# Optimization experiments

Measured on AMD Instinct MI355X. Metric: run time of the kernel, lower is better.

The kernel has to match this reference:

```python
import jax, jax.numpy as jnp
import numpy as np
import math

TAU_MEM = 20.0
ALPHA = math.exp(-1.0 / TAU_MEM)
BASE_THRESHOLD = 1.0


def setup_inputs() -> dict:
    key = jax.random.key(0)
    k1, k2, k3 = jax.random.split(key, 3)
    B, T, D, H = 32, 1024, 512, 512
    x = jax.random.normal(k1, (B, T, D), dtype=jnp.float32)
    # nn.Linear default init: U(-1/sqrt(D), 1/sqrt(D))
    bound = 1.0 / math.sqrt(D)
    W = jax.random.uniform(k2, (H, D), dtype=jnp.float32, minval=-bound, maxval=bound)
    b = jax.random.uniform(k3, (H,), dtype=jnp.float32, minval=-bound, maxval=bound)
    threshold_adapt = jnp.ones((H,), dtype=jnp.float32) * BASE_THRESHOLD
    return {"x": x, "W": W, "b": b, "threshold_adapt": threshold_adapt}


def reference(x, W, b, threshold_adapt):
    B, T, D = x.shape
    H = W.shape[0]
    # One batched GEMM instead of T small ones (same math as fc(x[:, t]) per step)
    xlin = jnp.einsum('btd,hd->bth', x, W) + b  # [B, T, H]
    xlin_t = jnp.transpose(xlin, (1, 0, 2))     # [T, B, H]

    def step(mem, xt):
        mem = ALPHA * mem + xt
        # torch std: unbiased (ddof=1), over hidden dim; B>1 branch
        mem_std = jnp.std(mem, axis=-1, keepdims=True, ddof=1)  # [B, 1]
        thr = threshold_adapt[None, :] + 0.1 * mem_std           # [B, H]
        spike = (mem >= thr).astype(mem.dtype)
        mem = mem * (1.0 - spike)
        return mem, spike

    mem0 = jnp.zeros((B, H), dtype=x.dtype)
    mem, spikes_t = jax.lax.scan(step, mem0, xlin_t)
    spikes = jnp.transpose(spikes_t, (1, 0, 2))  # [B, T, H]
    return spikes, mem
```

## Files before the change

### kernel.cpp

```cpp
#include <hip/hip_runtime.h>


#define ALPHA_F 0.95122942450071402f

constexpr int Bb = 32, T = 1024, D = 512, Hh = 512;
constexpr int M = Bb * T;
constexpr int NSCAN = 32;
constexpr int NBLOCKS = 256;
constexpr int NTILES = 512;

#define BM 128
#define BN 256
#define BK 16
#define LDA (BM + 4)
#define LDB (BN + 4)

template <int CTRL>
__device__ __forceinline__ float dpp_add(float v) {
  int s = __builtin_amdgcn_update_dpp(0, __builtin_bit_cast(int, v),
                                      CTRL, 0xF, 0xF, true);
  return v + __builtin_bit_cast(float, s);
}

__device__ __forceinline__ float dpp_reduce(float v) {
  v = dpp_add<0x111>(v);
  v = dpp_add<0x112>(v);
  v = dpp_add<0x114>(v);
  v = dpp_add<0x118>(v);
  v = dpp_add<0x142>(v);
  v = dpp_add<0x143>(v);
  return v;
}

__global__ void zero_ws_kernel(unsigned* ws) {
  if (threadIdx.x < 257) ws[threadIdx.x] = 0;
}

__global__ __launch_bounds__(512) void fused_kernel(
    const float* __restrict__ X,
    const float* __restrict__ W,
    const float* __restrict__ bias,
    const float* __restrict__ ta,
    float* out,
    float* memout,
    unsigned* ws)
{
  unsigned* prog = ws;
  unsigned* ticket = ws + 256;
  const int tid = threadIdx.x;

  if (blockIdx.x >= NSCAN) {
    __shared__ float As[BK][LDA];
    __shared__ float Bs[BK][LDB];
    __shared__ unsigned s_g;
    const int tm = tid >> 5;
    const int tn = tid & 31;
    for (;;) {
      __syncthreads();
      if (tid == 0)
        s_g = __hip_atomic_fetch_add(ticket, 1u, __ATOMIC_RELAXED,
                                     __HIP_MEMORY_SCOPE_AGENT);
      __syncthreads();
      const unsigned g = s_g;
      if (g >= NTILES) break;
      const int chg = (int)(g >> 6);
      const int idx = (int)(g & 63u);
      const int mt  = (idx >> 1) * 8 + chg;
      const int bn  = idx & 1;
      const int rowA = mt * BM;
      const int rowB = bn * BN;

      float acc[8][8];
#pragma unroll
      for (int i = 0; i < 8; ++i)
#pragma unroll
        for (int j = 0; j < 8; ++j) acc[i][j] = 0.f;

      for (int k0 = 0; k0 < D; k0 += BK) {
        __syncthreads();
        {
          const int r = tid >> 2;
          const int c4 = (tid & 3) << 2;
          float4 a = *(const float4*)(X + (size_t)(rowA + r) * D + k0 + c4);
          As[c4 + 0][r] = a.x; As[c4 + 1][r] = a.y;
          As[c4 + 2][r] = a.z; As[c4 + 3][r] = a.w;
        }
#pragma unroll
        for (int i = 0; i < 2; ++i) {
          const int f = tid + i * 512;
          const int r = f >> 2;
          const int c4 = (f & 3) << 2;
          float4 w = *(const float4*)(W + (size_t)(rowB + r) * D + k0 + c4);
          Bs[c4 + 0][r] = w.x; Bs[c4 + 1][r] = w.y;
          Bs[c4 + 2][r] = w.z; Bs[c4 + 3][r] = w.w;
        }
        __syncthreads();
#pragma unroll
        for (int k = 0; k < BK; ++k) {
          float4 a0 = *(const float4*)&As[k][tm * 4];
          float4 a1 = *(const float4*)&As[k][64 + tm * 4];
          float4 b0 = *(const float4*)&Bs[k][tn * 4];
          float4 b1 = *(const float4*)&Bs[k][128 + tn * 4];
          float av[8] = {a0.x, a0.y, a0.z, a0.w, a1.x, a1.y, a1.z, a1.w};
          float bv[8] = {b0.x, b0.y, b0.z, b0.w, b1.x, b1.y, b1.z, b1.w};
#pragma unroll
          for (int i = 0; i < 8; ++i)
#pragma unroll
            for (int j = 0; j < 8; ++j)
              acc[i][j] = fmaf(av[i], bv[j], acc[i][j]);
        }
      }

      const int c0 = rowB + tn * 4;
      const int c1 = rowB + 128 + tn * 4;
      float4 bb0 = *(const float4*)(bias + c0);
      float4 bb1 = *(const float4*)(bias + c1);
      float bc[8] = {bb0.x, bb0.y, bb0.z, bb0.w, bb1.x, bb1.y, bb1.z, bb1.w};
#pragma unroll
      for (int i = 0; i < 8; ++i) {
        const int r = rowA + ((i < 4) ? (tm * 4 + i) : (64 + tm * 4 + (i - 4)));
        float4 v0, v1;
        v0.x = acc[i][0] + bc[0]; v0.y = acc[i][1] + bc[1];
        v0.z = acc[i][2] + bc[2]; v0.w = acc[i][3] + bc[3];
        v1.x = acc[i][4] + bc[4]; v1.y = acc[i][5] + bc[5];
        v1.z = acc[i][6] + bc[6]; v1.w = acc[i][7] + bc[7];
        *(float4*)(out + (size_t)r * Hh + c0) = v0;
        *(float4*)(out + (size_t)r * Hh + c1) = v1;
      }
      __syncthreads();
      if (tid == 0)
        __hip_atomic_fetch_add(prog + mt, 1u, __ATOMIC_RELEASE,
                               __HIP_MEMORY_SCOPE_AGENT);
    }
    return;
  }

  if (tid >= 64) return;
  __builtin_amdgcn_s_setprio(3);

  const int b = blockIdx.x;
  const int lane = tid;
  float* base = out + (size_t)b * (size_t)(T * Hh);
  const int h0 = lane * 4;
  const int h1 = 256 + lane * 4;

  float4 tav0 = *(const float4*)(ta + h0);
  float4 tav1 = *(const float4*)(ta + h1);
  float tac[8] = {tav0.x, tav0.y, tav0.z, tav0.w,
                  tav1.x, tav1.y, tav1.z, tav1.w};

#define WAIT_CHUNK(idxc)                                                     \
  {                                                                          \
    unsigned* wp = prog + (idxc);                                            \
    while (__hip_atomic_load(wp, __ATOMIC_RELAXED,                           \
                             __HIP_MEMORY_SCOPE_AGENT) < 2u) {               \
      __builtin_amdgcn_s_sleep(2);                                           \
    }                                                                        \
    __builtin_amdgcn_fence(__ATOMIC_ACQUIRE, "agent");                       \
  }

  float4 pA0[8], pB0[8], pA1[8], pB1[8];
  float cc[8], mr[8];
  bool fire[8];
#pragma unroll
  for (int i = 0; i < 8; ++i) fire[i] = false;

#define LOAD1(NA, NB, u, t)                                                  \
  NA[u] = *(const float4*)(base + (size_t)(t) * Hh + h0);                    \
  NB[u] = *(const float4*)(base + (size_t)(t) * Hh + h1);

#define STEPX(CA, CB, u, t, NXA, NXB, SPEC)                                  \
  {                                                                          \
    const float xu_[8] = {CA[u].x, CA[u].y, CA[u].z, CA[u].w,                \
                          CB[u].x, CB[u].y, CB[u].z, CB[u].w};               \
    _Pragma("unroll")                                                        \
    for (int i = 0; i < 8; ++i) mr[i] = fire[i] ? xu_[i] : cc[i];            \
    float s_ = ((mr[0] + mr[1]) + (mr[2] + mr[3])) +                         \
               ((mr[4] + mr[5]) + (mr[6] + mr[7]));                          \
    float q_ = ((fmaf(mr[0], mr[0], mr[1] * mr[1])) +                        \
                (fmaf(mr[2], mr[2], mr[3] * mr[3]))) +                       \
               ((fmaf(mr[4], mr[4], mr[5] * mr[5])) +                        \
                (fmaf(mr[6], mr[6], mr[7] * mr[7])));                        \
    if (SPEC) {           \
      const float4 nxa_ = (NXA), nxb_ = (NXB);                               \
      const float xn_[8] = {nxa_.x, nxa_.y, nxa_.z, nxa_.w,                  \
                            nxb_.x, nxb_.y, nxb_.z, nxb_.w};                 \
      _Pragma("unroll")                                                      \
      for (int i = 0; i < 8; ++i) cc[i] = fmaf(ALPHA_F, mr[i], xn_[i]);      \
    }                                                                        \
    s_ = dpp_reduce(s_);                                                     \
    q_ = dpp_reduce(q_);                                                     \
    float var_ = fmaf(s_ * s_, -(1.0f / Hh), q_) * (1.0f / (Hh - 1));        \
    var_ = fmaxf(var_, 0.f);                                                 \
    float sdl_ = __builtin_amdgcn_sqrtf(var_);            \
    const float sd_ = __builtin_bit_cast(                                    \
        float,                                                               \
        __builtin_amdgcn_readlane(__builtin_bit_cast(int, sdl_), 63));       \
    float sp_[8];                                                            \
    _Pragma("unroll")                                                        \
    for (int i = 0; i < 8; ++i) {                                            \
      fire[i] = mr[i] >= fmaf(0.1f, sd_, tac[i]);                            \
      sp_[i] = fire[i] ? 1.f : 0.f;                                          \
    }                                                                        \
    *(float4*)(base + (size_t)(t) * Hh + h0) =                               \
        make_float4(sp_[0], sp_[1], sp_[2], sp_[3]);                         \
    *(float4*)(base + (size_t)(t) * Hh + h1) =                               \
        make_float4(sp_[4], sp_[5], sp_[6], sp_[7]);                         \
  }

#define GROUP(CA, CB, NA, NB, T0, PF, LASTG)                                 \
  {                                                                          \
    if (PF) {                                                                \
      LOAD1(NA, NB, 0, (T0) + 8)  LOAD1(NA, NB, 1, (T0) + 9)                 \
      LOAD1(NA, NB, 2, (T0) + 10) LOAD1(NA, NB, 3, (T0) + 11)                \
      LOAD1(NA, NB, 4, (T0) + 12) LOAD1(NA, NB, 5, (T0) + 13)                \
      LOAD1(NA, NB, 6, (T0) + 14) LOAD1(NA, NB, 7, (T0) + 15)                \
    }                                                                        \
    STEPX(CA, CB, 0, (T0) + 0, CA[1], CB[1], 1)                              \
    STEPX(CA, CB, 1, (T0) + 1, CA[2], CB[2], 1)                              \
    STEPX(CA, CB, 2, (T0) + 2, CA[3], CB[3], 1)                              \
    STEPX(CA, CB, 3, (T0) + 3, CA[4], CB[4], 1)                              \
    STEPX(CA, CB, 4, (T0) + 4, CA[5], CB[5], 1)                              \
    STEPX(CA, CB, 5, (T0) + 5, CA[6], CB[6], 1)                              \
    STEPX(CA, CB, 6, (T0) + 6, CA[7], CB[7], 1)                              \
    STEPX(CA, CB, 7, (T0) + 7, NA[0], NB[0], !(LASTG))                       \
  }

  WAIT_CHUNK(b * 8);
  LOAD1(pA0, pB0, 0, 0) LOAD1(pA0, pB0, 1, 1)
  LOAD1(pA0, pB0, 2, 2) LOAD1(pA0, pB0, 3, 3)
  LOAD1(pA0, pB0, 4, 4) LOAD1(pA0, pB0, 5, 5)
  LOAD1(pA0, pB0, 6, 6) LOAD1(pA0, pB0, 7, 7)
  cc[0] = pA0[0].x; cc[1] = pA0[0].y; cc[2] = pA0[0].z; cc[3] = pA0[0].w;
  cc[4] = pB0[0].x; cc[5] = pB0[0].y; cc[6] = pB0[0].z; cc[7] = pB0[0].w;

  for (int gp = 0; gp < 63; ++gp) {
    const int t0 = gp << 4;
    GROUP(pA0, pB0, pA1, pB1, t0, true, false)
    if ((gp & 7) == 7) WAIT_CHUNK(b * 8 + ((t0 + 16) >> 7));
    GROUP(pA1, pB1, pA0, pB0, t0 + 8, true, false)
  }
  GROUP(pA0, pB0, pA1, pB1, 1008, true, false)
  GROUP(pA1, pB1, pA0, pB0, 1016, false, true)

#undef GROUP
#undef STEPX
#undef LOAD1
#undef WAIT_CHUNK

  float mf[8];
#pragma unroll
  for (int i = 0; i < 8; ++i) mf[i] = fire[i] ? 0.f : mr[i];
  *(float4*)(memout + (size_t)b * Hh + h0) = make_float4(mf[0], mf[1], mf[2], mf[3]);
  *(float4*)(memout + (size_t)b * Hh + h1) = make_float4(mf[4], mf[5], mf[6], mf[7]);
}

__global__ __launch_bounds__(256) void gemm_kernel(
    const float* __restrict__ X, const float* __restrict__ W,
    const float* __restrict__ bias, float* __restrict__ out) {
  const int bn = blockIdx.x, bm = blockIdx.y;
  __shared__ float As[BK][BM + 4];
  __shared__ float Bs[BK][BM + 4];
  const int tid = threadIdx.x, tm = tid >> 4, tn = tid & 15;
  float acc[8][8];
#pragma unroll
  for (int i = 0; i < 8; ++i)
#pragma unroll
    for (int j = 0; j < 8; ++j) acc[i][j] = 0.f;
  const int rowA = bm * BM, rowB = bn * BM;
  for (int k0 = 0; k0 < D; k0 += BK) {
    __syncthreads();
#pragma unroll
    for (int i = 0; i < 2; ++i) {
      const int f = tid * 2 + i, r = f >> 2, c4 = (f & 3) << 2;
      float4 a = *(const float4*)(X + (size_t)(rowA + r) * D + k0 + c4);
      As[c4 + 0][r] = a.x; As[c4 + 1][r] = a.y;
      As[c4 + 2][r] = a.z; As[c4 + 3][r] = a.w;
      float4 w = *(const float4*)(W + (size_t)(rowB + r) * D + k0 + c4);
      Bs[c4 + 0][r] = w.x; Bs[c4 + 1][r] = w.y;
      Bs[c4 + 2][r] = w.z; Bs[c4 + 3][r] = w.w;
    }
    __syncthreads();
#pragma unroll
    for (int k = 0; k < BK; ++k) {
      float4 a0 = *(const float4*)&As[k][tm * 4];
      float4 a1 = *(const float4*)&As[k][64 + tm * 4];
      float4 b0 = *(const float4*)&Bs[k][tn * 4];
      float4 b1 = *(const float4*)&Bs[k][64 + tn * 4];
      float av[8] = {a0.x, a0.y, a0.z, a0.w, a1.x, a1.y, a1.z, a1.w};
      float bv[8] = {b0.x, b0.y, b0.z, b0.w, b1.x, b1.y, b1.z, b1.w};
#pragma unroll
      for (int i = 0; i < 8; ++i)
#pragma unroll
        for (int j = 0; j < 8; ++j)
          acc[i][j] = fmaf(av[i], bv[j], acc[i][j]);
    }
  }
  const int c0 = rowB + tn * 4, c1 = rowB + 64 + tn * 4;
  float4 bb0 = *(const float4*)(bias + c0);
  float4 bb1 = *(const float4*)(bias + c1);
  float bc[8] = {bb0.x, bb0.y, bb0.z, bb0.w, bb1.x, bb1.y, bb1.z, bb1.w};
#pragma unroll
  for (int i = 0; i < 8; ++i) {
    const int r = rowA + ((i < 4) ? (tm * 4 + i) : (64 + tm * 4 + (i - 4)));
    float4 v0, v1;
    v0.x = acc[i][0] + bc[0]; v0.y = acc[i][1] + bc[1];
    v0.z = acc[i][2] + bc[2]; v0.w = acc[i][3] + bc[3];
    v1.x = acc[i][4] + bc[4]; v1.y = acc[i][5] + bc[5];
    v1.z = acc[i][6] + bc[6]; v1.w = acc[i][7] + bc[7];
    *(float4*)(out + (size_t)r * Hh + c0) = v0;
    *(float4*)(out + (size_t)r * Hh + c1) = v1;
  }
}

__global__ __launch_bounds__(64) void scan_kernel(
    float* __restrict__ xs, const float* __restrict__ ta,
    float* __restrict__ memout) {
  const int b = blockIdx.x, lane = threadIdx.x;
  float* base = xs + (size_t)b * (size_t)(T * Hh);
  const int h0 = lane * 4, h1 = 256 + lane * 4;
  float4 tav0 = *(const float4*)(ta + h0);
  float4 tav1 = *(const float4*)(ta + h1);
  float tac[8] = {tav0.x, tav0.y, tav0.z, tav0.w,
                  tav1.x, tav1.y, tav1.z, tav1.w};
  float4 pa[4], pb[4];
#pragma unroll
  for (int u = 0; u < 4; ++u) {
    pa[u] = *(const float4*)(base + (size_t)u * Hh + h0);
    pb[u] = *(const float4*)(base + (size_t)u * Hh + h1);
  }
  float xc[8], cc[8], mr[8];
  bool fire[8];
  {
    const float4 a = pa[0], bq = pb[0];
    xc[0] = a.x; xc[1] = a.y; xc[2] = a.z; xc[3] = a.w;
    xc[4] = bq.x; xc[5] = bq.y; xc[6] = bq.z; xc[7] = bq.w;
  }
#pragma unroll
  for (int i = 0; i < 8; ++i) { cc[i] = xc[i]; fire[i] = false; }
#pragma unroll 4
  for (int t = 0; t < T; ++t) {
    const int u = t & 3;
    if (t + 4 < T) {
      pa[u] = *(const float4*)(base + (size_t)(t + 4) * Hh + h0);
      pb[u] = *(const float4*)(base + (size_t)(t + 4) * Hh + h1);
    }
#pragma unroll
    for (int i = 0; i < 8; ++i) mr[i] = fire[i] ? xc[i] : cc[i];
    float s = ((mr[0] + mr[1]) + (mr[2] + mr[3])) +
              ((mr[4] + mr[5]) + (mr[6] + mr[7]));
    float q = ((mr[0] * mr[0] + mr[1] * mr[1]) +
               (mr[2] * mr[2] + mr[3] * mr[3])) +
              ((mr[4] * mr[4] + mr[5] * mr[5]) +
               (mr[6] * mr[6] + mr[7] * mr[7]));
    {
      const float4 na = pa[(u + 1) & 3];
      const float4 nb = pb[(u + 1) & 3];
      xc[0] = na.x; xc[1] = na.y; xc[2] = na.z; xc[3] = na.w;
      xc[4] = nb.x; xc[5] = nb.y; xc[6] = nb.z; xc[7] = nb.w;
#pragma unroll
      for (int i = 0; i < 8; ++i) cc[i] = fmaf(ALPHA_F, mr[i], xc[i]);
    }
    s = dpp_reduce(s);
    q = dpp_reduce(q);
    float var = fmaxf((q - s * s * (1.0f / Hh)) * (1.0f / (Hh - 1)), 0.f);
    float sdl = __builtin_amdgcn_sqrtf(var);
    const float sd = __builtin_bit_cast(
        float, __builtin_amdgcn_readlane(__builtin_bit_cast(int, sdl), 63));
    float sp[8];
#pragma unroll
    for (int i = 0; i < 8; ++i) {
      fire[i] = mr[i] >= fmaf(0.1f, sd, tac[i]);
      sp[i] = fire[i] ? 1.f : 0.f;
    }
    *(float4*)(base + (size_t)t * Hh + h0) = make_float4(sp[0], sp[1], sp[2], sp[3]);
    *(float4*)(base + (size_t)t * Hh + h1) = make_float4(sp[4], sp[5], sp[6], sp[7]);
  }
  float mf[8];
#pragma unroll
  for (int i = 0; i < 8; ++i) mf[i] = fire[i] ? 0.f : mr[i];
  *(float4*)(memout + (size_t)b * Hh + h0) = make_float4(mf[0], mf[1], mf[2], mf[3]);
  *(float4*)(memout + (size_t)b * Hh + h1) = make_float4(mf[4], mf[5], mf[6], mf[7]);
}

extern "C" void kernel_launch(void* const* d_in, const int* in_sizes, int n_in,
                              void* d_out, int out_size, void* d_ws,
                              size_t ws_size, hipStream_t stream) {
  const float* x    = (const float*)d_in[0];
  const float* W    = (const float*)d_in[1];
  const float* bias = (const float*)d_in[2];
  const float* ta   = (const float*)d_in[3];

  float* out    = (float*)d_out;
  float* spikes = out;
  float* memout = out + (size_t)Bb * T * Hh;

  if (ws_size >= 257 * sizeof(unsigned)) {
    unsigned* ws = (unsigned*)d_ws;
    zero_ws_kernel<<<dim3(1), dim3(512), 0, stream>>>(ws);
    fused_kernel<<<dim3(NBLOCKS), dim3(512), 0, stream>>>(
        x, W, bias, ta, spikes, memout, ws);
  } else {
    dim3 ggrid(Hh / 128, M / BM);
    gemm_kernel<<<ggrid, dim3(256), 0, stream>>>(x, W, bias, spikes);
    scan_kernel<<<dim3(Bb), dim3(64), 0, stream>>>(spikes, ta, memout);
  }
}
```

Measured before the change: 324.8 us.

## Shrink GEMM tiles to 128x128 with 256-thread blocks and more worker blocks

The fused GEMM+scan kernel now uses 128x128 output tiles computed by 256-thread blocks instead of 128x256 tiles on 512 threads. The grid grows from 256 to 512 blocks, with blocks 256-287 exiting immediately. Each M-chunk now needs four completion signals before the scan consumes it. The goal is more concurrent GEMM workers, better occupancy and finer-grained producer/consumer overlap with the scan. The cost is less reuse per tile and more atomic signalling.

```diff
diff --git a/kernel.cpp b/kernel.cpp
--- a/kernel.cpp
+++ b/kernel.cpp
@@ -5,15 +5,12 @@
 
 constexpr int Bb = 32, T = 1024, D = 512, Hh = 512;
 constexpr int M = Bb * T;
-constexpr int NSCAN = 32;
-constexpr int NBLOCKS = 256;
-constexpr int NTILES = 512;
+constexpr int NBLOCKS = 512;
+constexpr int NTILES = (M / 128) * (Hh / 128);
+constexpr int SIG_PER_CHUNK = 4;
 
 #define BM 128
-#define BN 256
 #define BK 16
-#define LDA (BM + 4)
-#define LDB (BN + 4)
 
 template <int CTRL>
 __device__ __forceinline__ float dpp_add(float v) {
@@ -36,7 +33,7 @@
   if (threadIdx.x < 257) ws[threadIdx.x] = 0;
 }
 
-__global__ __launch_bounds__(512) void fused_kernel(
+__global__ __launch_bounds__(256) void fused_kernel(
     const float* __restrict__ X,
     const float* __restrict__ W,
     const float* __restrict__ bias,
@@ -48,13 +45,17 @@
   unsigned* prog = ws;
   unsigned* ticket = ws + 256;
   const int tid = threadIdx.x;
-
-  if (blockIdx.x >= NSCAN) {
-    __shared__ float As[BK][LDA];
-    __shared__ float Bs[BK][LDB];
+  const int bid = (int)blockIdx.x;
+
+  if (bid >= 256 && bid < 288) return;
+
+  if (bid >= 32) {
+    __shared__ float As[BK][BM + 4];
+    __shared__ float Bs[BK][BM + 4];
     __shared__ unsigned s_g;
-    const int tm = tid >> 5;
-    const int tn = tid & 31;
+    const int tm = tid >> 4;
+    const int tn = tid & 15;
+
     for (;;) {
       __syncthreads();
       if (tid == 0)
@@ -62,13 +63,14 @@
                                      __HIP_MEMORY_SCOPE_AGENT);
       __syncthreads();
       const unsigned g = s_g;
-      if (g >= NTILES) break;
-      const int chg = (int)(g >> 6);
-      const int idx = (int)(g & 63u);
-      const int mt  = (idx >> 1) * 8 + chg;
-      const int bn  = idx & 1;
-      const int rowA = mt * BM;
-      const int rowB = bn * BN;
+      if (g >= (unsigned)NTILES) break;
+      const int ch  = (int)(g >> 7);
+      const int idx = (int)(g & 127u);
+      const int b   = idx >> 2;
+      const int bn  = idx & 3;
+      const int bmt = b * 8 + ch;
+      const int rowA = bmt * BM;
+      const int rowB = bn * BM;
 
       float acc[8][8];
 #pragma unroll
@@ -78,18 +80,14 @@
 
       for (int k0 = 0; k0 < D; k0 += BK) {
         __syncthreads();
-        {
-          const int r = tid >> 2;
-          const int c4 = (tid & 3) << 2;
+#pragma unroll
+        for (int i = 0; i < 2; ++i) {
+          const int f = tid * 2 + i;
+          const int r = f >> 2;
+          const int c4 = (f & 3) << 2;
           float4 a = *(const float4*)(X + (size_t)(rowA + r) * D + k0 + c4);
           As[c4 + 0][r] = a.x; As[c4 + 1][r] = a.y;
           As[c4 + 2][r] = a.z; As[c4 + 3][r] = a.w;
-        }
-#pragma unroll
-        for (int i = 0; i < 2; ++i) {
-          const int f = tid + i * 512;
-          const int r = f >> 2;
-          const int c4 = (f & 3) << 2;
           float4 w = *(const float4*)(W + (size_t)(rowB + r) * D + k0 + c4);
           Bs[c4 + 0][r] = w.x; Bs[c4 + 1][r] = w.y;
           Bs[c4 + 2][r] = w.z; Bs[c4 + 3][r] = w.w;
@@ -100,7 +98,7 @@
           float4 a0 = *(const float4*)&As[k][tm * 4];
           float4 a1 = *(const float4*)&As[k][64 + tm * 4];
           float4 b0 = *(const float4*)&Bs[k][tn * 4];
-          float4 b1 = *(const float4*)&Bs[k][128 + tn * 4];
+          float4 b1 = *(const float4*)&Bs[k][64 + tn * 4];
           float av[8] = {a0.x, a0.y, a0.z, a0.w, a1.x, a1.y, a1.z, a1.w};
           float bv[8] = {b0.x, b0.y, b0.z, b0.w, b1.x, b1.y, b1.z, b1.w};
 #pragma unroll
@@ -112,7 +110,7 @@
       }
 
       const int c0 = rowB + tn * 4;
-      const int c1 = rowB + 128 + tn * 4;
+      const int c1 = rowB + 64 + tn * 4;
       float4 bb0 = *(const float4*)(bias + c0);
       float4 bb1 = *(const float4*)(bias + c1);
       float bc[8] = {bb0.x, bb0.y, bb0.z, bb0.w, bb1.x, bb1.y, bb1.z, bb1.w};
@@ -129,7 +127,7 @@
       }
       __syncthreads();
       if (tid == 0)
-        __hip_atomic_fetch_add(prog + mt, 1u, __ATOMIC_RELEASE,
+        __hip_atomic_fetch_add(prog + bmt, 1u, __ATOMIC_RELEASE,
                                __HIP_MEMORY_SCOPE_AGENT);
     }
     return;
@@ -138,7 +136,7 @@
   if (tid >= 64) return;
   __builtin_amdgcn_s_setprio(3);
 
-  const int b = blockIdx.x;
+  const int b = bid;
   const int lane = tid;
   float* base = out + (size_t)b * (size_t)(T * Hh);
   const int h0 = lane * 4;
@@ -153,7 +151,8 @@
   {                                                                          \
     unsigned* wp = prog + (idxc);                                            \
     while (__hip_atomic_load(wp, __ATOMIC_RELAXED,                           \
-                             __HIP_MEMORY_SCOPE_AGENT) < 2u) {               \
+                             __HIP_MEMORY_SCOPE_AGENT) <                     \
+           (unsigned)SIG_PER_CHUNK) {                                        \
       __builtin_amdgcn_s_sleep(2);                                           \
     }                                                                        \
     __builtin_amdgcn_fence(__ATOMIC_ACQUIRE, "agent");                       \
@@ -398,7 +397,7 @@
   if (ws_size >= 257 * sizeof(unsigned)) {
     unsigned* ws = (unsigned*)d_ws;
     zero_ws_kernel<<<dim3(1), dim3(512), 0, stream>>>(ws);
-    fused_kernel<<<dim3(NBLOCKS), dim3(512), 0, stream>>>(
+    fused_kernel<<<dim3(NBLOCKS), dim3(256), 0, stream>>>(
         x, W, bias, ta, spikes, memout, ws);
   } else {
     dim3 ggrid(Hh / 128, M / BM);
```

Measured after the change: 318.0 us. -2.1%, faster.
